# Kernel tuning notes

Measured on AMD Instinct MI355X. Metric: run time of the kernel, lower is better.

The kernel has to match this reference:

```python
import jax, jax.numpy as jnp
import numpy as np

N_NODES = 4096
N_EDGES = 16384
D_IN = 128
HID = 1024


def _linear_params(key, fan_in, fan_out):
    kw, kb = jax.random.split(key)
    bound = 1.0 / np.sqrt(fan_in)
    W = jax.random.uniform(kw, (fan_in, fan_out), jnp.float32, -bound, bound)
    b = jax.random.uniform(kb, (fan_out,), jnp.float32, -bound, bound)
    return W, b


def setup_inputs() -> dict:
    key = jax.random.key(0)
    ks = jax.random.split(key, 10)
    H = jax.random.normal(ks[0], (N_NODES, D_IN), jnp.float32)
    e = jax.random.uniform(ks[1], (N_NODES,), jnp.float32)
    # true incidence matrices: one-hot source/destination node per edge
    src = jax.random.randint(ks[2], (N_EDGES,), 0, N_NODES)
    dst = jax.random.randint(ks[3], (N_EDGES,), 0, N_NODES)
    Ro = jax.nn.one_hot(src, N_NODES, dtype=jnp.float32)  # [E, N]
    Ri = jax.nn.one_hot(dst, N_NODES, dtype=jnp.float32)  # [E, N]
    W1, b1 = _linear_params(ks[4], 3 * D_IN, HID)
    W2, b2 = _linear_params(ks[5], HID, HID)
    W3, b3 = _linear_params(ks[6], HID, HID // 2)
    W4, b4 = _linear_params(ks[7], HID // 2, HID // 4)
    W5, b5 = _linear_params(ks[8], HID // 4, 1)
    return {"H": H, "Ro": Ro, "Ri": Ri, "e": e,
            "W1": W1, "b1": b1, "W2": W2, "b2": b2, "W3": W3, "b3": b3,
            "W4": W4, "b4": b4, "W5": W5, "b5": b5}


def reference(H, Ro, Ri, e, W1, b1, W2, b2, W3, b3, W4, b4, W5, b5):
    eH = e[:, None] * H                      # [N, D]
    Ho = Ri.T @ (Ro @ eH)                    # aggregate over edges -> [N, D]
    Hi = Ro.T @ (Ri @ eH)                    # [N, D]
    x = jnp.concatenate([Ho, H, Hi], axis=1)  # [N, 3D]
    x = jnp.tanh(x @ W1 + b1)
    x = jnp.tanh(x @ W2 + b2)
    x = jnp.tanh(x @ W3 + b3)
    x = jnp.tanh(x @ W4 + b4)
    return jax.nn.sigmoid(x @ W5 + b5)       # [N, 1]
```

## Files before the change

### kernel.cpp

```cpp
#include <hip/hip_runtime.h>
#include <hip/hip_bf16.h>
#include <math.h>

#define N_NODES 4096
#define N_EDGES 16384
#define D_IN 128
#define HID 1024

typedef short s8v __attribute__((ext_vector_type(8)));
typedef float f4v __attribute__((ext_vector_type(4)));

__device__ __forceinline__ unsigned short f2b(float v) {
    union { float f; unsigned int u; } c; c.f = v;
    unsigned int u = c.u + 0x7fffu + ((c.u >> 16) & 1u);
    return (unsigned short)(u >> 16);
}
__device__ __forceinline__ float b2f(unsigned short b) {
    union { unsigned int u; float f; } c; c.u = ((unsigned int)b) << 16;
    return c.f;
}
__device__ __forceinline__ void glds16(const unsigned short* g, unsigned short* l) {
    __builtin_amdgcn_global_load_lds(
        (const __attribute__((address_space(1))) void*)g,
        (__attribute__((address_space(3))) void*)l, 16, 0, 0);
}

__global__ void extract_idx(const float* __restrict__ Ro, const float* __restrict__ Ri,
                            int* __restrict__ src, int* __restrict__ dst) {
    __shared__ int found;
    int b = blockIdx.x;
    const float* rowp;
    int* outp;
    if (b < N_EDGES) { rowp = Ro + (size_t)b * N_NODES; outp = src + b; }
    else             { rowp = Ri + (size_t)(b - N_EDGES) * N_NODES; outp = dst + (b - N_EDGES); }
    int t = threadIdx.x;
    if (t == 0) found = 0;
    __syncthreads();
    const float4* r4 = (const float4*)rowp;
    for (int i = 0; i < 4; ++i) {
        int c = t + i * 256;
        float4 v = r4[c];
        if (v.x != 0.0f || v.y != 0.0f || v.z != 0.0f || v.w != 0.0f) {
            int idx = c * 4 + (v.x != 0.0f ? 0 : v.y != 0.0f ? 1 : v.z != 0.0f ? 2 : 3);
            *outp = idx;
            found = 1;
        }
        __syncthreads();
        if (found) break;
    }
}

__global__ void scatter(const int* __restrict__ src, const int* __restrict__ dst,
                        const float* __restrict__ H, const float* __restrict__ e,
                        float* __restrict__ xf) {
    int i = blockIdx.x * 256 + threadIdx.x;
    int ed = i >> 7, j = i & 127;
    int s = src[ed], d = dst[ed];
    atomicAdd(&xf[(size_t)d * 256 + j],       e[s] * H[(size_t)s * 128 + j]);
    atomicAdd(&xf[(size_t)s * 256 + 128 + j], e[d] * H[(size_t)d * 128 + j]);
}

__global__ void cvt_x(const float* __restrict__ xf, const float* __restrict__ H,
                      unsigned short* __restrict__ xb) {
    int n = blockIdx.x, c = threadIdx.x;
    float v;
    if (c < 128)       v = xf[(size_t)n * 256 + c];
    else if (c < 256)  v = H[(size_t)n * 128 + c - 128];
    else               v = xf[(size_t)n * 256 + c - 128];
    xb[(size_t)n * 384 + c] = f2b(v);
}

__global__ void wtrans_all(const float* __restrict__ W1, unsigned short* __restrict__ wt1,
                           const float* __restrict__ W2, unsigned short* __restrict__ wt2,
                           const float* __restrict__ W3, unsigned short* __restrict__ wt3,
                           const float* __restrict__ W4, unsigned short* __restrict__ wt4,
                           const float* __restrict__ W5, unsigned short* __restrict__ wt5) {
    int b = blockIdx.x, t = threadIdx.x;
    const float* W; unsigned short* WT; int K, N, tb;
    if (b < 384)       { W = W1; WT = wt1; K = 384;  N = 1024; tb = b; }
    else if (b < 1408) { W = W2; WT = wt2; K = 1024; N = 1024; tb = b - 384; }
    else if (b < 1920) { W = W3; WT = wt3; K = 1024; N = 512;  tb = b - 1408; }
    else if (b < 2048) { W = W4; WT = wt4; K = 512;  N = 256;  tb = b - 1920; }
    else { wt5[t] = f2b(W5[t]); return; }

    __shared__ float tile[32][33];
    int ntx = N >> 5;
    int tk = tb / ntx, tn = tb - tk * ntx;
    int tr = t >> 5, tc = t & 31;
#pragma unroll
    for (int i = 0; i < 4; ++i)
        tile[tr + i * 8][tc] = W[(size_t)(tk * 32 + tr + i * 8) * N + tn * 32 + tc];
    __syncthreads();
#pragma unroll
    for (int i = 0; i < 4; ++i)
        WT[(size_t)(tn * 32 + tr + i * 8) * K + tk * 32 + tc] = f2b(tile[tc][tr + i * 8]);
}

template<int BM, int BN>
__global__ __launch_bounds__(256)
void gemm_tanh(const unsigned short* __restrict__ A, const unsigned short* __restrict__ BT,
               const float* __restrict__ bias, unsigned short* __restrict__ C,
               int M, int N, int K) {
    constexpr int BK = 32;
    constexpr int MI = BM / 32;
    constexpr int NI = BN / 32;
    constexpr int AITER = BM / 64;
    constexpr int BITER = BN / 64;
    __shared__ unsigned short As[BM * BK];
    __shared__ unsigned short Bs[BN * BK];
    int t = threadIdx.x;
    int l = t & 63, w = t >> 6;
    int wm = w >> 1, wn = w & 1;
    int q = l >> 4, r16 = l & 15;
    int m0 = blockIdx.y * BM, n0 = blockIdx.x * BN;

    f4v acc[MI][NI] = {};

    for (int k0 = 0; k0 < K; k0 += BK) {
        __syncthreads();
#pragma unroll
        for (int i = 0; i < AITER; ++i) {
            int c = (i * 4 + w) * 64 + l;
            int row = c >> 2, ko = (c & 3) * 8;
            glds16(&A[(size_t)(m0 + row) * K + k0 + ko], &As[c * 8]);
        }
#pragma unroll
        for (int i = 0; i < BITER; ++i) {
            int c = (i * 4 + w) * 64 + l;
            int row = c >> 2, ko = (c & 3) * 8;
            glds16(&BT[(size_t)(n0 + row) * K + k0 + ko], &Bs[c * 8]);
        }
        __syncthreads();
        s8v a[MI], b[NI];
#pragma unroll
        for (int mi = 0; mi < MI; ++mi)
            a[mi] = *(const s8v*)&As[(wm * (BM / 2) + mi * 16 + r16) * BK + q * 8];
#pragma unroll
        for (int ni = 0; ni < NI; ++ni)
            b[ni] = *(const s8v*)&Bs[(wn * (BN / 2) + ni * 16 + r16) * BK + q * 8];
#pragma unroll
        for (int mi = 0; mi < MI; ++mi)
#pragma unroll
            for (int ni = 0; ni < NI; ++ni)
                acc[mi][ni] = __builtin_amdgcn_mfma_f32_16x16x32_bf16(a[mi], b[ni], acc[mi][ni], 0, 0, 0);
    }

#pragma unroll
    for (int mi = 0; mi < MI; ++mi) {
#pragma unroll
        for (int ni = 0; ni < NI; ++ni) {
            int col = n0 + wn * (BN / 2) + ni * 16 + r16;
            float bv = bias[col];
#pragma unroll
            for (int r = 0; r < 4; ++r) {
                int row = m0 + wm * (BM / 2) + mi * 16 + q * 4 + r;
                C[(size_t)row * N + col] = f2b(tanhf(acc[mi][ni][r] + bv));
            }
        }
    }
}

__global__ void layer5(const unsigned short* __restrict__ h4, const unsigned short* __restrict__ w5,
                       const float* __restrict__ b5, float* __restrict__ out) {
    int row = blockIdx.x * 4 + (threadIdx.x >> 6);
    int l = threadIdx.x & 63;
    const ushort4 hv = *(const ushort4*)(h4 + (size_t)row * 256 + l * 4);
    const ushort4 wv = *(const ushort4*)(w5 + l * 4);
    float s = b2f(hv.x) * b2f(wv.x) + b2f(hv.y) * b2f(wv.y)
            + b2f(hv.z) * b2f(wv.z) + b2f(hv.w) * b2f(wv.w);
#pragma unroll
    for (int off = 32; off > 0; off >>= 1) s += __shfl_down(s, off);
    if (l == 0) out[row] = 1.0f / (1.0f + expf(-(s + b5[0])));
}

extern "C" void kernel_launch(void* const* d_in, const int* in_sizes, int n_in,
                              void* d_out, int out_size, void* d_ws, size_t ws_size,
                              hipStream_t stream) {
    const float* H  = (const float*)d_in[0];
    const float* Ro = (const float*)d_in[1];
    const float* Ri = (const float*)d_in[2];
    const float* e  = (const float*)d_in[3];
    const float* W1 = (const float*)d_in[4];  const float* b1 = (const float*)d_in[5];
    const float* W2 = (const float*)d_in[6];  const float* b2 = (const float*)d_in[7];
    const float* W3 = (const float*)d_in[8];  const float* b3 = (const float*)d_in[9];
    const float* W4 = (const float*)d_in[10]; const float* b4 = (const float*)d_in[11];
    const float* W5 = (const float*)d_in[12]; const float* b5 = (const float*)d_in[13];
    float* out = (float*)d_out;

    char* p = (char*)d_ws;
    auto alloc = [&](size_t bytes) -> void* {
        void* r = (void*)p;
        p += (bytes + 255) & ~(size_t)255;
        return r;
    };
    int*   src = (int*)  alloc(N_EDGES * 4);
    int*   dst = (int*)  alloc(N_EDGES * 4);
    float* xf  = (float*)alloc((size_t)N_NODES * 256 * 4);
    unsigned short* xb  = (unsigned short*)alloc((size_t)N_NODES * 384 * 2);
    unsigned short* h1  = (unsigned short*)alloc((size_t)N_NODES * HID * 2);
    unsigned short* h2  = (unsigned short*)alloc((size_t)N_NODES * HID * 2);
    unsigned short* h3  = (unsigned short*)alloc((size_t)N_NODES * (HID / 2) * 2);
    unsigned short* h4  = (unsigned short*)alloc((size_t)N_NODES * (HID / 4) * 2);
    unsigned short* wt1 = (unsigned short*)alloc((size_t)HID * 384 * 2);
    unsigned short* wt2 = (unsigned short*)alloc((size_t)HID * HID * 2);
    unsigned short* wt3 = (unsigned short*)alloc((size_t)(HID / 2) * HID * 2);
    unsigned short* wt4 = (unsigned short*)alloc((size_t)(HID / 4) * (HID / 2) * 2);
    unsigned short* wt5 = (unsigned short*)alloc((size_t)(HID / 4) * 2);

    hipMemsetAsync(xf, 0, (size_t)N_NODES * 256 * 4, stream);

    extract_idx<<<2 * N_EDGES, 256, 0, stream>>>(Ro, Ri, src, dst);

    wtrans_all<<<2049, 256, 0, stream>>>(W1, wt1, W2, wt2, W3, wt3, W4, wt4, W5, wt5);

    scatter<<<(N_EDGES * 128) / 256, 256, 0, stream>>>(src, dst, H, e, xf);

    cvt_x<<<N_NODES, 384, 0, stream>>>(xf, H, xb);

    gemm_tanh<128, 64><<<dim3(HID / 64, N_NODES / 128), 256, 0, stream>>>(xb, wt1, b1, h1, N_NODES, HID, 384);
    gemm_tanh<128, 64><<<dim3(HID / 64, N_NODES / 128), 256, 0, stream>>>(h1, wt2, b2, h2, N_NODES, HID, HID);
    gemm_tanh<128, 64><<<dim3((HID / 2) / 64, N_NODES / 128), 256, 0, stream>>>(h2, wt3, b3, h3, N_NODES, HID / 2, HID);
    gemm_tanh<64, 64><<<dim3((HID / 4) / 64, N_NODES / 64), 256, 0, stream>>>(h3, wt4, b4, h4, N_NODES, HID / 4, HID / 2);

    layer5<<<N_NODES / 4, 256, 0, stream>>>(h4, wt5, b5, out);
}
```

Measured before the change: 597.3 us.

## Fuse index extraction with scatter, fold bf16 conversion into layer-1 GEMM

```diff
diff --git a/kernel.cpp b/kernel.cpp
--- a/kernel.cpp
+++ b/kernel.cpp
@@ -25,49 +25,53 @@
         (__attribute__((address_space(3))) void*)l, 16, 0, 0);
 }
 
-__global__ void extract_idx(const float* __restrict__ Ro, const float* __restrict__ Ri,
-                            int* __restrict__ src, int* __restrict__ dst) {
-    __shared__ int found;
-    int b = blockIdx.x;
-    const float* rowp;
-    int* outp;
-    if (b < N_EDGES) { rowp = Ro + (size_t)b * N_NODES; outp = src + b; }
-    else             { rowp = Ri + (size_t)(b - N_EDGES) * N_NODES; outp = dst + (b - N_EDGES); }
-    int t = threadIdx.x;
-    if (t == 0) found = 0;
-    __syncthreads();
-    const float4* r4 = (const float4*)rowp;
-    for (int i = 0; i < 4; ++i) {
-        int c = t + i * 256;
-        float4 v = r4[c];
-        if (v.x != 0.0f || v.y != 0.0f || v.z != 0.0f || v.w != 0.0f) {
-            int idx = c * 4 + (v.x != 0.0f ? 0 : v.y != 0.0f ? 1 : v.z != 0.0f ? 2 : 3);
-            *outp = idx;
-            found = 1;
-        }
-        __syncthreads();
-        if (found) break;
-    }
-}
-
-__global__ void scatter(const int* __restrict__ src, const int* __restrict__ dst,
-                        const float* __restrict__ H, const float* __restrict__ e,
-                        float* __restrict__ xf) {
-    int i = blockIdx.x * 256 + threadIdx.x;
-    int ed = i >> 7, j = i & 127;
-    int s = src[ed], d = dst[ed];
-    atomicAdd(&xf[(size_t)d * 256 + j],       e[s] * H[(size_t)s * 128 + j]);
-    atomicAdd(&xf[(size_t)s * 256 + 128 + j], e[d] * H[(size_t)d * 128 + j]);
-}
-
-__global__ void cvt_x(const float* __restrict__ xf, const float* __restrict__ H,
-                      unsigned short* __restrict__ xb) {
-    int n = blockIdx.x, c = threadIdx.x;
-    float v;
-    if (c < 128)       v = xf[(size_t)n * 256 + c];
-    else if (c < 256)  v = H[(size_t)n * 128 + c - 128];
-    else               v = xf[(size_t)n * 256 + c - 128];
-    xb[(size_t)n * 384 + c] = f2b(v);
+__global__ void extract_scatter(const float* __restrict__ Ro, const float* __restrict__ Ri,
+                                const float* __restrict__ H, const float* __restrict__ e,
+                                float* __restrict__ xf) {
+    int edge = (blockIdx.x * 256 + threadIdx.x) >> 6;
+    int l = threadIdx.x & 63;
+    const float4* ro4 = (const float4*)(Ro + (size_t)edge * N_NODES);
+    const float4* ri4 = (const float4*)(Ri + (size_t)edge * N_NODES);
+    int src = -1, dst = -1;
+    for (int it = 0; it < 16; ++it) {
+        if (src < 0) {
+            float4 v = ro4[it * 64 + l];
+            bool hit = (v.x != 0.0f) | (v.y != 0.0f) | (v.z != 0.0f) | (v.w != 0.0f);
+            unsigned long long m = __ballot(hit);
+            if (m) {
+                int fl = __ffsll((long long)m) - 1;
+                int idx = 0;
+                if (hit) idx = (it * 64 + l) * 4 + (v.x != 0.0f ? 0 : v.y != 0.0f ? 1 : v.z != 0.0f ? 2 : 3);
+                src = __shfl(idx, fl);
+            }
+        }
+        if (dst < 0) {
+            float4 v = ri4[it * 64 + l];
+            bool hit = (v.x != 0.0f) | (v.y != 0.0f) | (v.z != 0.0f) | (v.w != 0.0f);
+            unsigned long long m = __ballot(hit);
+            if (m) {
+                int fl = __ffsll((long long)m) - 1;
+                int idx = 0;
+                if (hit) idx = (it * 64 + l) * 4 + (v.x != 0.0f ? 0 : v.y != 0.0f ? 1 : v.z != 0.0f ? 2 : 3);
+                dst = __shfl(idx, fl);
+            }
+        }
+        if (src >= 0 && dst >= 0) break;
+    }
+    float es = e[src], ed = e[dst];
+    if (l < 32) {
+        int f = l * 4;
+        float4 h = *(const float4*)(H + (size_t)src * 128 + f);
+        float* o = xf + (size_t)dst * 256 + f;
+        atomicAdd(o + 0, es * h.x); atomicAdd(o + 1, es * h.y);
+        atomicAdd(o + 2, es * h.z); atomicAdd(o + 3, es * h.w);
+    } else {
+        int f = (l - 32) * 4;
+        float4 h = *(const float4*)(H + (size_t)dst * 128 + f);
+        float* o = xf + (size_t)src * 256 + 128 + f;
+        atomicAdd(o + 0, ed * h.x); atomicAdd(o + 1, ed * h.y);
+        atomicAdd(o + 2, ed * h.z); atomicAdd(o + 3, ed * h.w);
+    }
 }
 
 __global__ void wtrans_all(const float* __restrict__ W1, unsigned short* __restrict__ wt1,
@@ -96,16 +100,83 @@
         WT[(size_t)(tn * 32 + tr + i * 8) * K + tk * 32 + tc] = f2b(tile[tc][tr + i * 8]);
 }
 
+#define L1_BM 128
+#define L1_BN 64
+__global__ __launch_bounds__(256)
+void gemm1(const float* __restrict__ xf, const float* __restrict__ H,
+           const unsigned short* __restrict__ BT, const float* __restrict__ bias,
+           unsigned short* __restrict__ C) {
+    constexpr int BK = 32, K = 384, N = HID;
+    constexpr int MI = L1_BM / 32, NI = L1_BN / 32;
+    __shared__ unsigned short As[L1_BM * BK];
+    __shared__ unsigned short Bs[L1_BN * BK];
+    int t = threadIdx.x;
+    int l = t & 63, w = t >> 6;
+    int wm = w >> 1, wn = w & 1;
+    int q = l >> 4, r16 = l & 15;
+    int m0 = blockIdx.y * L1_BM, n0 = blockIdx.x * L1_BN;
+
+    f4v acc[MI][NI] = {};
+
+    for (int k0 = 0; k0 < K; k0 += BK) {
+        __syncthreads();
+#pragma unroll
+        for (int i = 0; i < 2; ++i) {
+            int c = i * 256 + t;
+            int row = c >> 2, ko = (c & 3) * 8;
+            const float* sp;
+            if (k0 < 128)      sp = xf + (size_t)(m0 + row) * 256 + k0 + ko;
+            else if (k0 < 256) sp = H + (size_t)(m0 + row) * 128 + (k0 - 128) + ko;
+            else               sp = xf + (size_t)(m0 + row) * 256 + (k0 - 128) + ko;
+            float4 f0 = *(const float4*)sp, f1 = *(const float4*)(sp + 4);
+            s8v pk;
+            pk[0] = (short)f2b(f0.x); pk[1] = (short)f2b(f0.y);
+            pk[2] = (short)f2b(f0.z); pk[3] = (short)f2b(f0.w);
+            pk[4] = (short)f2b(f1.x); pk[5] = (short)f2b(f1.y);
+            pk[6] = (short)f2b(f1.z); pk[7] = (short)f2b(f1.w);
+            *(s8v*)&As[c * 8] = pk;
+        }
+        {
+            int c = w * 64 + l;
+            int row = c >> 2, ko = (c & 3) * 8;
+            glds16(&BT[(size_t)(n0 + row) * K + k0 + ko], &Bs[c * 8]);
+        }
+        __syncthreads();
+        s8v a[MI], b[NI];
+#pragma unroll
+        for (int mi = 0; mi < MI; ++mi)
+            a[mi] = *(const s8v*)&As[(wm * (L1_BM / 2) + mi * 16 + r16) * BK + q * 8];
+#pragma unroll
+        for (int ni = 0; ni < NI; ++ni)
+            b[ni] = *(const s8v*)&Bs[(wn * (L1_BN / 2) + ni * 16 + r16) * BK + q * 8];
+#pragma unroll
+        for (int mi = 0; mi < MI; ++mi)
+#pragma unroll
+            for (int ni = 0; ni < NI; ++ni)
+                acc[mi][ni] = __builtin_amdgcn_mfma_f32_16x16x32_bf16(a[mi], b[ni], acc[mi][ni], 0, 0, 0);
+    }
+#pragma unroll
+    for (int mi = 0; mi < MI; ++mi)
+#pragma unroll
+        for (int ni = 0; ni < NI; ++ni) {
+            int col = n0 + wn * (L1_BN / 2) + ni * 16 + r16;
+            float bv = bias[col];
+#pragma unroll
+            for (int r = 0; r < 4; ++r) {
+                int row = m0 + wm * (L1_BM / 2) + mi * 16 + q * 4 + r;
+                C[(size_t)row * N + col] = f2b(tanhf(acc[mi][ni][r] + bv));
+            }
+        }
+}
+
 template<int BM, int BN>
 __global__ __launch_bounds__(256)
 void gemm_tanh(const unsigned short* __restrict__ A, const unsigned short* __restrict__ BT,
                const float* __restrict__ bias, unsigned short* __restrict__ C,
                int M, int N, int K) {
     constexpr int BK = 32;
-    constexpr int MI = BM / 32;
-    constexpr int NI = BN / 32;
-    constexpr int AITER = BM / 64;
-    constexpr int BITER = BN / 64;
+    constexpr int MI = BM / 32, NI = BN / 32;
+    constexpr int AITER = BM / 64, BITER = BN / 64;
     __shared__ unsigned short As[BM * BK];
     __shared__ unsigned short Bs[BN * BK];
     int t = threadIdx.x;
@@ -144,9 +215,8 @@
             for (int ni = 0; ni < NI; ++ni)
                 acc[mi][ni] = __builtin_amdgcn_mfma_f32_16x16x32_bf16(a[mi], b[ni], acc[mi][ni], 0, 0, 0);
     }
-
-#pragma unroll
-    for (int mi = 0; mi < MI; ++mi) {
+#pragma unroll
+    for (int mi = 0; mi < MI; ++mi)
 #pragma unroll
         for (int ni = 0; ni < NI; ++ni) {
             int col = n0 + wn * (BN / 2) + ni * 16 + r16;
@@ -157,7 +227,6 @@
                 C[(size_t)row * N + col] = f2b(tanhf(acc[mi][ni][r] + bv));
             }
         }
-    }
 }
 
 __global__ void layer5(const unsigned short* __restrict__ h4, const unsigned short* __restrict__ w5,
@@ -193,10 +262,7 @@
         p += (bytes + 255) & ~(size_t)255;
         return r;
     };
-    int*   src = (int*)  alloc(N_EDGES * 4);
-    int*   dst = (int*)  alloc(N_EDGES * 4);
-    float* xf  = (float*)alloc((size_t)N_NODES * 256 * 4);
-    unsigned short* xb  = (unsigned short*)alloc((size_t)N_NODES * 384 * 2);
+    float* xf = (float*)alloc((size_t)N_NODES * 256 * 4);
     unsigned short* h1  = (unsigned short*)alloc((size_t)N_NODES * HID * 2);
     unsigned short* h2  = (unsigned short*)alloc((size_t)N_NODES * HID * 2);
     unsigned short* h3  = (unsigned short*)alloc((size_t)N_NODES * (HID / 2) * 2);
@@ -209,17 +275,13 @@
 
     hipMemsetAsync(xf, 0, (size_t)N_NODES * 256 * 4, stream);
 
-    extract_idx<<<2 * N_EDGES, 256, 0, stream>>>(Ro, Ri, src, dst);
+    extract_scatter<<<N_EDGES / 4, 256, 0, stream>>>(Ro, Ri, H, e, xf);
 
     wtrans_all<<<2049, 256, 0, stream>>>(W1, wt1, W2, wt2, W3, wt3, W4, wt4, W5, wt5);
 
-    scatter<<<(N_EDGES * 128) / 256, 256, 0, stream>>>(src, dst, H, e, xf);
-
-    cvt_x<<<N_NODES, 384, 0, stream>>>(xf, H, xb);
-
-    gemm_tanh<128, 64><<<dim3(HID / 64, N_NODES / 128), 256, 0, stream>>>(xb, wt1, b1, h1, N_NODES, HID, 384);
+    gemm1<<<dim3(HID / L1_BN, N_NODES / L1_BM), 256, 0, stream>>>(xf, H, wt1, b1, h1);
     gemm_tanh<128, 64><<<dim3(HID / 64, N_NODES / 128), 256, 0, stream>>>(h1, wt2, b2, h2, N_NODES, HID, HID);
-    gemm_tanh<128, 64><<<dim3((HID / 2) / 64, N_NODES / 128), 256, 0, stream>>>(h2, wt3, b3, h3, N_NODES, HID / 2, HID);
+    gemm_tanh<64, 64><<<dim3((HID / 2) / 64, N_NODES / 64), 256, 0, stream>>>(h2, wt3, b3, h3, N_NODES, HID / 2, HID);
     gemm_tanh<64, 64><<<dim3((HID / 4) / 64, N_NODES / 64), 256, 0, stream>>>(h3, wt4, b4, h4, N_NODES, HID / 4, HID / 2);
 
     layer5<<<N_NODES / 4, 256, 0, stream>>>(h4, wt5, b5, out);
```

Result: faster. 576.9 us (-3.4%).
